# Kernel optimization log

Hardware: AMD Instinct MI355X
Metric: run time of the kernel (lower is better)

## Reference

```python
import jax, jax.numpy as jnp
import numpy as np

EPS = 1e-6
K_HOPS = 2  # SGConv K


def setup_inputs() -> dict:
    key = jax.random.key(0)
    k1, k2, k3, k4 = jax.random.split(key, 4)
    B, Kk, C, T = 32, 8, 64, 250
    E, H = 4096, 128
    x = jax.random.normal(k1, (B, Kk, C, T), dtype=jnp.float32)
    edge_index = jax.random.randint(k2, (2, E), 0, C, dtype=jnp.int64)
    edge_weights = jax.random.uniform(k3, (E,), dtype=jnp.float32)
    W = jax.random.normal(k4, (H, Kk * T), dtype=jnp.float32) * 0.02
    b = jnp.zeros((H,), dtype=jnp.float32)
    return {"x": x, "edge_index": edge_index, "edge_weights": edge_weights, "W": W, "b": b}


def reference(x, edge_index, edge_weights, W, b):
    B, Kk, C, T = x.shape
    N = C  # nodes
    x = x.reshape(B, N, Kk * T)  # (B, N, F)

    # clamp non-positive edge weights to epsilon (mirrors in-place .data clamp)
    w = jnp.where(edge_weights <= 0, EPS, edge_weights)

    # gcn_norm with self loops (fill value 1.0)
    src, dst = edge_index[0], edge_index[1]
    loop = jnp.arange(N, dtype=edge_index.dtype)
    src = jnp.concatenate([src, loop])
    dst = jnp.concatenate([dst, loop])
    w = jnp.concatenate([w, jnp.ones((N,), w.dtype)])
    deg = jnp.zeros((N,), w.dtype).at[dst].add(w)
    dinv = jnp.where(deg > 0, deg ** -0.5, jnp.zeros_like(deg))
    norm = dinv[src] * w * dinv[dst]  # (E+N,)

    # K hops of gather -> weight -> scatter-add aggregation
    for _ in range(K_HOPS):
        msg = x[:, src, :] * norm[None, :, None]        # (B, E+N, F)
        x = jnp.zeros_like(x).at[:, dst, :].add(msg)    # (B, N, F)

    # final linear: y = x @ W^T + b
    return jnp.einsum('bnf,hf->bnh', x, W) + b
```

## Files before the change

kernel.cpp:

```cpp
#include <hip/hip_runtime.h>
#include <hip/hip_bf16.h>

#define EPSW 1e-6f

typedef __attribute__((ext_vector_type(4))) float floatx4;
typedef __attribute__((ext_vector_type(4))) unsigned int uintx4;
typedef __attribute__((ext_vector_type(8))) short shortx8;

__device__ __forceinline__ unsigned short f2bf(float f) {
    unsigned int u = __float_as_uint(f);
    u = (u + 0x7fffu + ((u >> 16) & 1u)) >> 16;
    return (unsigned short)u;
}

__device__ __forceinline__ unsigned int pk2(float lo, float hi) {
    return (unsigned int)f2bf(lo) | ((unsigned int)f2bf(hi) << 16);
}

__device__ __forceinline__ shortx8 pk8s(floatx4 a, floatx4 b) {
    union { uintx4 u; shortx8 s; } r;
    r.u.x = pk2(a.x, a.y); r.u.y = pk2(a.z, a.w);
    r.u.z = pk2(b.x, b.y); r.u.w = pk2(b.z, b.w);
    return r.s;
}

__global__ __launch_bounds__(256) void gemm_mt(
        const float* __restrict__ x,
        const float* __restrict__ W,
        const int* __restrict__ ei,
        const float* __restrict__ ew,
        float* __restrict__ zp,
        float* __restrict__ Mt) {
    __shared__ float sA[4224];
    const int bid = blockIdx.x;
    const int t   = threadIdx.x;

    if (bid >= 256) {
        const int bm = bid - 256;
        float* A    = sA;
        float* deg  = A + 4096;
        float* dinv = deg + 64;
        if (t < 64) deg[t] = 1.0f;
        for (int i = t; i < 4096; i += 256) A[i] = 0.0f;
        __syncthreads();
        const int* srcp = ei;
        const int* dstp = ei + 4096;
#pragma unroll
        for (int i = 0; i < 16; ++i) {
            const int e = i * 256 + t;
            float w = ew[e];
            w = (w <= 0.0f) ? EPSW : w;
            atomicAdd(&deg[dstp[e]], w);
        }
        __syncthreads();
        if (t < 64) dinv[t] = 1.0f / sqrtf(deg[t]);
        __syncthreads();
#pragma unroll
        for (int i = 0; i < 16; ++i) {
            const int e = i * 256 + t;
            float w = ew[e];
            w = (w <= 0.0f) ? EPSW : w;
            const int s = srcp[e], d = dstp[e];
            atomicAdd(&A[d * 64 + s], dinv[s] * w * dinv[d]);
        }
        if (t < 64) atomicAdd(&A[t * 64 + t], dinv[t] * dinv[t]);
        __syncthreads();
        const int c  = t & 63;
        const int rr = t >> 6;
        float s0 = 0.f, s1 = 0.f, s2 = 0.f, s3 = 0.f;
#pragma unroll 8
        for (int k = 0; k < 64; ++k) {
            const float akc = A[k * 64 + c];
            const float* an = A + (bm * 16 + rr * 4) * 64 + k;
            s0 += an[0]   * akc;
            s1 += an[64]  * akc;
            s2 += an[128] * akc;
            s3 += an[192] * akc;
        }
        float* mo = Mt + c * 64 + bm * 16 + rr * 4;
        mo[0] = s0; mo[1] = s1; mo[2] = s2; mo[3] = s3;
        return;
    }

    const int ks    = bid & 7;
    const int rtile = bid >> 3;
    const int rbase = rtile * 64;
    const int kbase = ks * 256;

    const int wave = t >> 6, lane = t & 63;
    const int m = lane & 15, q = lane >> 4;

    const float* xr[4];
    const float* wr[2];
#pragma unroll
    for (int rt = 0; rt < 4; ++rt)
        xr[rt] = x + (size_t)(rbase + rt * 16 + m) * 2000;
#pragma unroll
    for (int hh = 0; hh < 2; ++hh)
        wr[hh] = W + (size_t)((wave + hh * 4) * 16 + m) * 2000;

    floatx4 acc[4][2];
#pragma unroll
    for (int rt = 0; rt < 4; ++rt)
#pragma unroll
        for (int hh = 0; hh < 2; ++hh)
            acc[rt][hh] = (floatx4){0.f, 0.f, 0.f, 0.f};

    floatx4 fx[4][2][2];
    floatx4 fw[2][2][2];

#define LOADC(c)                                                              \
    {                                                                         \
        _Pragma("unroll")                                                     \
        for (int p_ = 0; p_ < 2; ++p_) {                                      \
            const int k_ = kbase + (c) * 64 + (p_ * 4 + q) * 8;               \
            if (k_ < 2000) {                                                  \
                _Pragma("unroll")                                             \
                for (int rt_ = 0; rt_ < 4; ++rt_) {                           \
                    fx[rt_][p_][0] = *(const floatx4*)(xr[rt_] + k_);         \
                    fx[rt_][p_][1] = *(const floatx4*)(xr[rt_] + k_ + 4);     \
                }                                                             \
                _Pragma("unroll")                                             \
                for (int hh_ = 0; hh_ < 2; ++hh_) {                           \
                    fw[hh_][p_][0] = *(const floatx4*)(wr[hh_] + k_);         \
                    fw[hh_][p_][1] = *(const floatx4*)(wr[hh_] + k_ + 4);     \
                }                                                             \
            } else {                                                          \
                _Pragma("unroll")                                             \
                for (int rt_ = 0; rt_ < 4; ++rt_)                             \
                    fx[rt_][p_][0] = fx[rt_][p_][1] =                         \
                        (floatx4){0.f, 0.f, 0.f, 0.f};                        \
                _Pragma("unroll")                                             \
                for (int hh_ = 0; hh_ < 2; ++hh_)                             \
                    fw[hh_][p_][0] = fw[hh_][p_][1] =                         \
                        (floatx4){0.f, 0.f, 0.f, 0.f};                        \
            }                                                                 \
        }                                                                     \
    }

    LOADC(0);
#pragma unroll
    for (int c = 0; c < 4; ++c) {
        shortx8 af[4][2], bf[2][2];
#pragma unroll
        for (int p = 0; p < 2; ++p) {
#pragma unroll
            for (int rt = 0; rt < 4; ++rt)
                af[rt][p] = pk8s(fx[rt][p][0], fx[rt][p][1]);
#pragma unroll
            for (int hh = 0; hh < 2; ++hh)
                bf[hh][p] = pk8s(fw[hh][p][0], fw[hh][p][1]);
        }
        if (c < 3) LOADC(c + 1);
#pragma unroll
        for (int p = 0; p < 2; ++p)
#pragma unroll
            for (int rt = 0; rt < 4; ++rt)
#pragma unroll
                for (int hh = 0; hh < 2; ++hh)
                    acc[rt][hh] = __builtin_amdgcn_mfma_f32_16x16x32_bf16(
                        af[rt][p], bf[hh][p], acc[rt][hh], 0, 0, 0);
    }
#undef LOADC

    float* zslice = zp + ((size_t)ks * 2048 + rbase) * 128;
#pragma unroll
    for (int rt = 0; rt < 4; ++rt)
#pragma unroll
        for (int hh = 0; hh < 2; ++hh) {
            const int h = (wave + hh * 4) * 16 + m;
#pragma unroll
            for (int v = 0; v < 4; ++v) {
                const int n = rt * 16 + q * 4 + v;
                zslice[n * 128 + h] = acc[rt][hh][v];
            }
        }
}

__global__ __launch_bounds__(256) void apply_M(const float* __restrict__ zp,
                                               const float* __restrict__ Mtg,
                                               const float* __restrict__ bias,
                                               float* __restrict__ y) {
    __shared__ float Ms[4096];
    __shared__ float zs[64][16];
    const int b  = blockIdx.x;
    const int hc = blockIdx.y;
    const int t  = threadIdx.x;
#pragma unroll
    for (int i = 0; i < 16; ++i) Ms[i * 256 + t] = Mtg[i * 256 + t];
#pragma unroll
    for (int i = 0; i < 4; ++i) {
        const int idx = i * 256 + t;
        const int mr = idx >> 4, hh = idx & 15;
        float s = 0.0f;
#pragma unroll
        for (int ks = 0; ks < 8; ++ks)
            s += zp[((size_t)ks * 2048 + b * 64 + mr) * 128 + hc * 16 + hh];
        zs[mr][hh] = s;
    }
    __syncthreads();
    const int h  = t & 15;
    const int n0 = (t >> 4) * 4;
    const float bv = bias[hc * 16 + h];
    float s0 = bv, s1 = bv, s2 = bv, s3 = bv;
#pragma unroll
    for (int mm = 0; mm < 64; ++mm) {
        const float zv = zs[mm][h];
        s0 += Ms[mm * 64 + n0 + 0] * zv;
        s1 += Ms[mm * 64 + n0 + 1] * zv;
        s2 += Ms[mm * 64 + n0 + 2] * zv;
        s3 += Ms[mm * 64 + n0 + 3] * zv;
    }
    float* yp = y + (size_t)b * 8192 + (size_t)n0 * 128 + hc * 16 + h;
    yp[0]   = s0;
    yp[128] = s1;
    yp[256] = s2;
    yp[384] = s3;
}

extern "C" void kernel_launch(void* const* d_in, const int* in_sizes, int n_in,
                              void* d_out, int out_size, void* d_ws, size_t ws_size,
                              hipStream_t stream) {
    const float* x    = (const float*)d_in[0];
    const int*   ei   = (const int*)d_in[1];
    const float* ew   = (const float*)d_in[2];
    const float* W    = (const float*)d_in[3];
    const float* bias = (const float*)d_in[4];
    float* y = (float*)d_out;

    float* zp = (float*)d_ws;
    float* Mt = zp + 2097152;

    gemm_mt<<<260, 256, 0, stream>>>(x, W, ei, ew, zp, Mt);
    apply_M<<<dim3(32, 8), 256, 0, stream>>>(zp, Mt, bias, y);
}
```

Measured before the change: 94.42 us.

## Fuse GEMM split-K reduction and M application into one kernel per batch/head-slice

Splits the propagation-matrix build into its own small kernel, and fuses the x@W^T GEMM with the 64x64 M application into one kernel. Each 512-thread block owns one batch and a 16-wide head slice, and its eight waves split K. Partial sums are reduced in LDS rather than written to a global split-K workspace and read back. This removes the 8 MB global partial-sum round trip, at the cost of recomputing loads of x across the 8 head slices and adding a dependent kernel launch before the GEMM.

```diff
diff --git a/kernel.cpp b/kernel.cpp
--- a/kernel.cpp
+++ b/kernel.cpp
@@ -24,198 +24,165 @@
     return r.s;
 }
 
-__global__ __launch_bounds__(256) void gemm_mt(
+__global__ __launch_bounds__(256) void mbuild(const int* __restrict__ ei,
+                                              const float* __restrict__ ew,
+                                              float* __restrict__ Mt) {
+    __shared__ float sA[4224];
+    const int bm = blockIdx.x;
+    const int t  = threadIdx.x;
+    float* A    = sA;
+    float* deg  = A + 4096;
+    float* dinv = deg + 64;
+    if (t < 64) deg[t] = 1.0f;
+    for (int i = t; i < 4096; i += 256) A[i] = 0.0f;
+    __syncthreads();
+    const int* srcp = ei;
+    const int* dstp = ei + 4096;
+#pragma unroll
+    for (int i = 0; i < 16; ++i) {
+        const int e = i * 256 + t;
+        float w = ew[e];
+        w = (w <= 0.0f) ? EPSW : w;
+        atomicAdd(&deg[dstp[e]], w);
+    }
+    __syncthreads();
+    if (t < 64) dinv[t] = 1.0f / sqrtf(deg[t]);
+    __syncthreads();
+#pragma unroll
+    for (int i = 0; i < 16; ++i) {
+        const int e = i * 256 + t;
+        float w = ew[e];
+        w = (w <= 0.0f) ? EPSW : w;
+        const int s = srcp[e], d = dstp[e];
+        atomicAdd(&A[d * 64 + s], dinv[s] * w * dinv[d]);
+    }
+    if (t < 64) atomicAdd(&A[t * 64 + t], dinv[t] * dinv[t]);
+    __syncthreads();
+    const int c  = t & 63;
+    const int rr = t >> 6;
+    float s0 = 0.f, s1 = 0.f, s2 = 0.f, s3 = 0.f;
+#pragma unroll 8
+    for (int k = 0; k < 64; ++k) {
+        const float akc = A[k * 64 + c];
+        const float* an = A + (bm * 16 + rr * 4) * 64 + k;
+        s0 += an[0]   * akc;
+        s1 += an[64]  * akc;
+        s2 += an[128] * akc;
+        s3 += an[192] * akc;
+    }
+    float* mo = Mt + c * 64 + bm * 16 + rr * 4;
+    mo[0] = s0; mo[1] = s1; mo[2] = s2; mo[3] = s3;
+}
+
+__global__ __launch_bounds__(512) void gcn_fused(
         const float* __restrict__ x,
         const float* __restrict__ W,
-        const int* __restrict__ ei,
-        const float* __restrict__ ew,
-        float* __restrict__ zp,
-        float* __restrict__ Mt) {
-    __shared__ float sA[4224];
-    const int bid = blockIdx.x;
-    const int t   = threadIdx.x;
-
-    if (bid >= 256) {
-        const int bm = bid - 256;
-        float* A    = sA;
-        float* deg  = A + 4096;
-        float* dinv = deg + 64;
-        if (t < 64) deg[t] = 1.0f;
-        for (int i = t; i < 4096; i += 256) A[i] = 0.0f;
-        __syncthreads();
-        const int* srcp = ei;
-        const int* dstp = ei + 4096;
-#pragma unroll
-        for (int i = 0; i < 16; ++i) {
-            const int e = i * 256 + t;
-            float w = ew[e];
-            w = (w <= 0.0f) ? EPSW : w;
-            atomicAdd(&deg[dstp[e]], w);
-        }
-        __syncthreads();
-        if (t < 64) dinv[t] = 1.0f / sqrtf(deg[t]);
-        __syncthreads();
-#pragma unroll
-        for (int i = 0; i < 16; ++i) {
-            const int e = i * 256 + t;
-            float w = ew[e];
-            w = (w <= 0.0f) ? EPSW : w;
-            const int s = srcp[e], d = dstp[e];
-            atomicAdd(&A[d * 64 + s], dinv[s] * w * dinv[d]);
-        }
-        if (t < 64) atomicAdd(&A[t * 64 + t], dinv[t] * dinv[t]);
-        __syncthreads();
-        const int c  = t & 63;
-        const int rr = t >> 6;
-        float s0 = 0.f, s1 = 0.f, s2 = 0.f, s3 = 0.f;
-#pragma unroll 8
-        for (int k = 0; k < 64; ++k) {
-            const float akc = A[k * 64 + c];
-            const float* an = A + (bm * 16 + rr * 4) * 64 + k;
-            s0 += an[0]   * akc;
-            s1 += an[64]  * akc;
-            s2 += an[128] * akc;
-            s3 += an[192] * akc;
-        }
-        float* mo = Mt + c * 64 + bm * 16 + rr * 4;
-        mo[0] = s0; mo[1] = s1; mo[2] = s2; mo[3] = s3;
-        return;
-    }
-
-    const int ks    = bid & 7;
-    const int rtile = bid >> 3;
-    const int rbase = rtile * 64;
-    const int kbase = ks * 256;
+        const float* __restrict__ Mtg,
+        const float* __restrict__ bias,
+        float* __restrict__ y) {
+    __shared__ __align__(16) float lds[8 * 1088 + 1088 + 4096];
+    float* zpart = lds;
+    float* zs    = lds + 8 * 1088;
+    float* Ms    = zs + 1088;
+
+    const int t     = threadIdx.x;
+    const int bid   = blockIdx.x;
+    const int hs    = bid >> 5;
+    const int batch = bid & 31;
+    const int rbase = batch * 64;
+    const int hbase = hs * 16;
 
     const int wave = t >> 6, lane = t & 63;
     const int m = lane & 15, q = lane >> 4;
 
-    const float* xr[4];
-    const float* wr[2];
+    const float* xr0 = x + (size_t)(rbase + m) * 2000;
+    const float* wr  = W + (size_t)(hbase + m) * 2000;
+
+    floatx4 acc[4];
+#pragma unroll
+    for (int rt = 0; rt < 4; ++rt) acc[rt] = (floatx4){0.f, 0.f, 0.f, 0.f};
+
+    floatx4 fA[3][4][2];
+    floatx4 fB[3][2];
+
+#define LOADK(i_)                                                             \
+    {                                                                         \
+        const int s_ = (i_) % 3;                                              \
+        const int c_ = wave + (i_) * 8;                      \
+        const int k_ = c_ * 32 + q * 8;                                       \
+        if (k_ < 2000) {                                                      \
+            _Pragma("unroll")                                                 \
+            for (int rt_ = 0; rt_ < 4; ++rt_) {                               \
+                const float* p_ = xr0 + rt_ * 32000 + k_;                     \
+                fA[s_][rt_][0] = *(const floatx4*)p_;                         \
+                fA[s_][rt_][1] = *(const floatx4*)(p_ + 4);                   \
+            }                                                                 \
+            fB[s_][0] = *(const floatx4*)(wr + k_);                           \
+            fB[s_][1] = *(const floatx4*)(wr + k_ + 4);                       \
+        } else {                                                              \
+            _Pragma("unroll")                                                 \
+            for (int rt_ = 0; rt_ < 4; ++rt_)                                 \
+                fA[s_][rt_][0] = fA[s_][rt_][1] =                             \
+                    (floatx4){0.f, 0.f, 0.f, 0.f};                            \
+            fB[s_][0] = fB[s_][1] = (floatx4){0.f, 0.f, 0.f, 0.f};            \
+        }                                                                     \
+    }
+
+    LOADK(0);
+    LOADK(1);
+#pragma unroll
+    for (int i = 0; i < 8; ++i) {
+        const int s = i % 3;
+        shortx8 af[4];
+#pragma unroll
+        for (int rt = 0; rt < 4; ++rt)
+            af[rt] = pk8s(fA[s][rt][0], fA[s][rt][1]);
+        const shortx8 bf = pk8s(fB[s][0], fB[s][1]);
+        if (i < 6) LOADK(i + 2);
+#pragma unroll
+        for (int rt = 0; rt < 4; ++rt)
+            acc[rt] = __builtin_amdgcn_mfma_f32_16x16x32_bf16(
+                af[rt], bf, acc[rt], 0, 0, 0);
+    }
+#undef LOADK
+
+    const floatx4 msr0 = *(const floatx4*)(Mtg + t * 8);
+    const floatx4 msr1 = *(const floatx4*)(Mtg + t * 8 + 4);
+
+    float* zw = zpart + wave * 1088;
 #pragma unroll
     for (int rt = 0; rt < 4; ++rt)
-        xr[rt] = x + (size_t)(rbase + rt * 16 + m) * 2000;
-#pragma unroll
-    for (int hh = 0; hh < 2; ++hh)
-        wr[hh] = W + (size_t)((wave + hh * 4) * 16 + m) * 2000;
-
-    floatx4 acc[4][2];
-#pragma unroll
-    for (int rt = 0; rt < 4; ++rt)
-#pragma unroll
-        for (int hh = 0; hh < 2; ++hh)
-            acc[rt][hh] = (floatx4){0.f, 0.f, 0.f, 0.f};
-
-    floatx4 fx[4][2][2];
-    floatx4 fw[2][2][2];
-
-#define LOADC(c)                                                              \
-    {                                                                         \
-        _Pragma("unroll")                                                     \
-        for (int p_ = 0; p_ < 2; ++p_) {                                      \
-            const int k_ = kbase + (c) * 64 + (p_ * 4 + q) * 8;               \
-            if (k_ < 2000) {                                                  \
-                _Pragma("unroll")                                             \
-                for (int rt_ = 0; rt_ < 4; ++rt_) {                           \
-                    fx[rt_][p_][0] = *(const floatx4*)(xr[rt_] + k_);         \
-                    fx[rt_][p_][1] = *(const floatx4*)(xr[rt_] + k_ + 4);     \
-                }                                                             \
-                _Pragma("unroll")                                             \
-                for (int hh_ = 0; hh_ < 2; ++hh_) {                           \
-                    fw[hh_][p_][0] = *(const floatx4*)(wr[hh_] + k_);         \
-                    fw[hh_][p_][1] = *(const floatx4*)(wr[hh_] + k_ + 4);     \
-                }                                                             \
-            } else {                                                          \
-                _Pragma("unroll")                                             \
-                for (int rt_ = 0; rt_ < 4; ++rt_)                             \
-                    fx[rt_][p_][0] = fx[rt_][p_][1] =                         \
-                        (floatx4){0.f, 0.f, 0.f, 0.f};                        \
-                _Pragma("unroll")                                             \
-                for (int hh_ = 0; hh_ < 2; ++hh_)                             \
-                    fw[hh_][p_][0] = fw[hh_][p_][1] =                         \
-                        (floatx4){0.f, 0.f, 0.f, 0.f};                        \
-            }                                                                 \
-        }                                                                     \
-    }
-
-    LOADC(0);
-#pragma unroll
-    for (int c = 0; c < 4; ++c) {
-        shortx8 af[4][2], bf[2][2];
-#pragma unroll
-        for (int p = 0; p < 2; ++p) {
-#pragma unroll
-            for (int rt = 0; rt < 4; ++rt)
-                af[rt][p] = pk8s(fx[rt][p][0], fx[rt][p][1]);
-#pragma unroll
-            for (int hh = 0; hh < 2; ++hh)
-                bf[hh][p] = pk8s(fw[hh][p][0], fw[hh][p][1]);
-        }
-        if (c < 3) LOADC(c + 1);
-#pragma unroll
-        for (int p = 0; p < 2; ++p)
-#pragma unroll
-            for (int rt = 0; rt < 4; ++rt)
-#pragma unroll
-                for (int hh = 0; hh < 2; ++hh)
-                    acc[rt][hh] = __builtin_amdgcn_mfma_f32_16x16x32_bf16(
-                        af[rt][p], bf[hh][p], acc[rt][hh], 0, 0, 0);
-    }
-#undef LOADC
-
-    float* zslice = zp + ((size_t)ks * 2048 + rbase) * 128;
-#pragma unroll
-    for (int rt = 0; rt < 4; ++rt)
-#pragma unroll
-        for (int hh = 0; hh < 2; ++hh) {
-            const int h = (wave + hh * 4) * 16 + m;
-#pragma unroll
-            for (int v = 0; v < 4; ++v) {
-                const int n = rt * 16 + q * 4 + v;
-                zslice[n * 128 + h] = acc[rt][hh][v];
-            }
-        }
-}
-
-__global__ __launch_bounds__(256) void apply_M(const float* __restrict__ zp,
-                                               const float* __restrict__ Mtg,
-                                               const float* __restrict__ bias,
-                                               float* __restrict__ y) {
-    __shared__ float Ms[4096];
-    __shared__ float zs[64][16];
-    const int b  = blockIdx.x;
-    const int hc = blockIdx.y;
-    const int t  = threadIdx.x;
-#pragma unroll
-    for (int i = 0; i < 16; ++i) Ms[i * 256 + t] = Mtg[i * 256 + t];
-#pragma unroll
-    for (int i = 0; i < 4; ++i) {
-        const int idx = i * 256 + t;
-        const int mr = idx >> 4, hh = idx & 15;
+#pragma unroll
+        for (int v = 0; v < 4; ++v)
+            zw[(rt * 16 + q * 4 + v) * 17 + m] = acc[rt][v];
+    __syncthreads();
+
+#pragma unroll
+    for (int i = 0; i < 2; ++i) {
+        const int idx = i * 512 + t;
+        const int row = idx >> 4, hh = idx & 15;
         float s = 0.0f;
 #pragma unroll
-        for (int ks = 0; ks < 8; ++ks)
-            s += zp[((size_t)ks * 2048 + b * 64 + mr) * 128 + hc * 16 + hh];
-        zs[mr][hh] = s;
-    }
-    __syncthreads();
+        for (int w = 0; w < 8; ++w) s += zpart[w * 1088 + row * 17 + hh];
+        zs[row * 17 + hh] = s;
+    }
+    *(floatx4*)(Ms + t * 8)     = msr0;
+    *(floatx4*)(Ms + t * 8 + 4) = msr1;
+    __syncthreads();
+
     const int h  = t & 15;
-    const int n0 = (t >> 4) * 4;
-    const float bv = bias[hc * 16 + h];
-    float s0 = bv, s1 = bv, s2 = bv, s3 = bv;
-#pragma unroll
+    const int n0 = (t >> 4) * 2;
+    float s0 = 0.0f, s1 = 0.0f;
+#pragma unroll 8
     for (int mm = 0; mm < 64; ++mm) {
-        const float zv = zs[mm][h];
-        s0 += Ms[mm * 64 + n0 + 0] * zv;
+        const float zv = zs[mm * 17 + h];
+        s0 += Ms[mm * 64 + n0]     * zv;
         s1 += Ms[mm * 64 + n0 + 1] * zv;
-        s2 += Ms[mm * 64 + n0 + 2] * zv;
-        s3 += Ms[mm * 64 + n0 + 3] * zv;
-    }
-    float* yp = y + (size_t)b * 8192 + (size_t)n0 * 128 + hc * 16 + h;
-    yp[0]   = s0;
-    yp[128] = s1;
-    yp[256] = s2;
-    yp[384] = s3;
+    }
+    const float bv = bias[hbase + h];
+    float* yp = y + (size_t)batch * 8192 + (size_t)n0 * 128 + hbase + h;
+    yp[0]   = bv + s0;
+    yp[128] = bv + s1;
 }
 
 extern "C" void kernel_launch(void* const* d_in, const int* in_sizes, int n_in,
@@ -228,9 +195,8 @@
     const float* bias = (const float*)d_in[4];
     float* y = (float*)d_out;
 
-    float* zp = (float*)d_ws;
-    float* Mt = zp + 2097152;
-
-    gemm_mt<<<260, 256, 0, stream>>>(x, W, ei, ew, zp, Mt);
-    apply_M<<<dim3(32, 8), 256, 0, stream>>>(zp, Mt, bias, y);
-}
+    float* Mt = (float*)d_ws;
+
+    mbuild<<<4, 256, 0, stream>>>(ei, ew, Mt);
+    gcn_fused<<<256, 512, 0, stream>>>(x, W, Mt, bias, y);
+}
```

New measurement: 98.52 us. 4.3% more time.
